# Performance work log

Hardware: AMD Instinct MI355X
Metric: run time of the kernel (lower is better)

The kernel has to match this reference:

```python
import jax, jax.numpy as jnp
import numpy as np

NEG_INF = -1e6

def setup_inputs() -> dict:
    key = jax.random.key(0)
    ks = jax.random.split(key, 7)
    B, Q, K, D, H = 16, 64, 1024, 256, 128
    return {
        "queries": jax.random.normal(ks[0], (B, Q, D), dtype=jnp.float32),
        "keys": jax.random.normal(ks[1], (B, K, D), dtype=jnp.float32),
        "values": jax.random.normal(ks[2], (B, K, D), dtype=jnp.float32),
        "valid_lens": jax.random.randint(ks[3], (B,), 1, K + 1, dtype=jnp.int32),
        "W_q": jax.random.normal(ks[4], (D, H), dtype=jnp.float32) * (1.0 / np.sqrt(D)),
        "W_k": jax.random.normal(ks[5], (D, H), dtype=jnp.float32) * (1.0 / np.sqrt(D)),
        "w_v": jax.random.normal(ks[6], (H,), dtype=jnp.float32) * (1.0 / np.sqrt(H)),
    }

def reference(queries, keys, values, valid_lens, W_q, W_k, w_v):
    # project: [B,Q,H], [B,K,H]
    q = jnp.einsum('bqd,dh->bqh', queries, W_q)
    k = jnp.einsum('bkd,dh->bkh', keys, W_k)
    # broadcast add -> tanh -> score: [B,Q,K]
    features = jnp.tanh(q[:, :, None, :] + k[:, None, :, :])  # [B,Q,K,H]
    scores = jnp.einsum('bqkh,h->bqk', features, w_v)
    # masked softmax over key axis (valid_lens per batch)
    K_len = keys.shape[1]
    mask = jnp.arange(K_len)[None, None, :] < valid_lens[:, None, None]  # [B,1,K]
    scores = jnp.where(mask, scores, NEG_INF)
    attn = jax.nn.softmax(scores, axis=-1)
    # weighted sum of values: [B,Q,Dv]  (dropout p=0 -> identity)
    return jnp.einsum('bqk,bkd->bqd', attn, values)
```

## Files before the change

### kernel.cpp

```cpp
#include <hip/hip_runtime.h>

#define DDIM 256
#define HDIM 128
#define KLEN 1024
#define SCL 2.8853900817779268f

__global__ __launch_bounds__(256) void proj_kernel(
    const float* __restrict__ queries, const float* __restrict__ keys,
    const float* __restrict__ W_q, const float* __restrict__ W_k,
    float* __restrict__ Eq, float* __restrict__ Ek)
{
    __shared__ union {
        float w[64][64];
        float t[64][33];
    } sm;

    int tid = threadIdx.x;
    int hg = tid & 31;
    int rg = tid >> 5;
    int blk = blockIdx.x;

    const float* in; const float* W; int row0, hbase, b = 0, kc0 = 0; bool iskey;
    if (blk < 1024) {
        iskey = true;
        int xcd = blk & 7, s = blk >> 3;
        b = ((s >> 6) << 3) | xcd;
        int r6 = s & 63;
        kc0   = (r6 >> 1) * 32;
        hbase = (r6 & 1) << 6;
        row0  = b * KLEN + kc0;
        in = keys; W = W_k;
    } else {
        iskey = false;
        int qrb = blk - 1024;
        row0  = (qrb >> 1) * 32;
        hbase = (qrb & 1) << 6;
        in = queries; W = W_q;
    }

    float2 acc[4];
    #pragma unroll
    for (int j = 0; j < 4; j++) acc[j] = make_float2(0.f, 0.f);

    for (int dt = 0; dt < DDIM; dt += 64) {
        __syncthreads();
        #pragma unroll
        for (int i = 0; i < 4; i++) {
            int idx = tid + 256 * i;
            int dd = idx >> 4, hl = (idx & 15) << 2;
            *(float4*)(&sm.w[dd][hl]) =
                *(const float4*)(W + (size_t)(dt + dd) * HDIM + hbase + hl);
        }
        __syncthreads();

        #pragma unroll 4
        for (int d4 = 0; d4 < 64; d4 += 4) {
            float2 wr[4];
            #pragma unroll
            for (int dd = 0; dd < 4; dd++)
                wr[dd] = *(const float2*)(&sm.w[d4 + dd][hg << 1]);
            #pragma unroll
            for (int j = 0; j < 4; j++) {
                float4 a = *(const float4*)(in + (size_t)(row0 + rg * 4 + j) * DDIM + dt + d4);
                acc[j].x = fmaf(a.x, wr[0].x, acc[j].x); acc[j].y = fmaf(a.x, wr[0].y, acc[j].y);
                acc[j].x = fmaf(a.y, wr[1].x, acc[j].x); acc[j].y = fmaf(a.y, wr[1].y, acc[j].y);
                acc[j].x = fmaf(a.z, wr[2].x, acc[j].x); acc[j].y = fmaf(a.z, wr[2].y, acc[j].y);
                acc[j].x = fmaf(a.w, wr[3].x, acc[j].x); acc[j].y = fmaf(a.w, wr[3].y, acc[j].y);
            }
        }
    }

    if (!iskey) {
        #pragma unroll
        for (int j = 0; j < 4; j++) {
            float2 o = make_float2(__builtin_amdgcn_exp2f(SCL * acc[j].x),
                                   __builtin_amdgcn_exp2f(SCL * acc[j].y));
            *(float2*)(Eq + (size_t)(row0 + rg * 4 + j) * HDIM + hbase + (hg << 1)) = o;
        }
    } else {
        __syncthreads();
        #pragma unroll
        for (int j = 0; j < 4; j++) {
            sm.t[(hg << 1) + 0][rg * 4 + j] = __builtin_amdgcn_exp2f(SCL * acc[j].x);
            sm.t[(hg << 1) + 1][rg * 4 + j] = __builtin_amdgcn_exp2f(SCL * acc[j].y);
        }
        __syncthreads();
        float* dst = Ek + (size_t)b * HDIM * KLEN + (size_t)hbase * KLEN + kc0;
        #pragma unroll
        for (int i = 0; i < 2; i++) {
            int idx = tid + 256 * i;
            int hh = idx >> 3, c = (idx & 7) << 2;
            float4 o = make_float4(sm.t[hh][c], sm.t[hh][c + 1],
                                   sm.t[hh][c + 2], sm.t[hh][c + 3]);
            *(float4*)(dst + (size_t)hh * KLEN + c) = o;
        }
    }
}

__global__ __launch_bounds__(512) void score_kernel(
    const float* __restrict__ Eq, const float* __restrict__ Ek,
    const float* __restrict__ w_v, const int* __restrict__ valid_lens,
    float* __restrict__ p)
{
    __shared__ float4 eqw[HDIM];
    __shared__ float red0[8], red1[8];

    int tid = threadIdx.x, lane = tid & 63, wav = tid >> 6;
    int blk = blockIdx.x;
    int xcd = blk & 7, s = blk >> 3;
    int b = ((s >= 32) ? 8 : 0) + xcd;
    int qp = s & 31;
    int bq0 = b * 64 + qp * 2;
    int vlen = valid_lens[b];

    if (tid < HDIM) {
        float w2 = -2.0f * w_v[tid];
        eqw[tid] = make_float4(Eq[(size_t)bq0 * HDIM + tid],
                               Eq[(size_t)(bq0 + 1) * HDIM + tid], w2, 0.f);
    }
    __syncthreads();

    int k0 = tid << 1;
    float s00 = -1e30f, s01 = -1e30f, s10 = -1e30f, s11 = -1e30f;
    if (k0 < vlen) {
        const float* ekp = Ek + (size_t)b * HDIM * KLEN + k0;
        float a00 = 0.f, a01 = 0.f, a10 = 0.f, a11 = 0.f;
        #pragma unroll 4
        for (int h = 0; h < HDIM; h++) {
            float2 ek = *(const float2*)(ekp + (size_t)h * KLEN);
            float4 e  = eqw[h];
            a00 = fmaf(e.z, __builtin_amdgcn_rcpf(fmaf(e.x, ek.x, 1.f)), a00);
            a01 = fmaf(e.z, __builtin_amdgcn_rcpf(fmaf(e.x, ek.y, 1.f)), a01);
            a10 = fmaf(e.z, __builtin_amdgcn_rcpf(fmaf(e.y, ek.x, 1.f)), a10);
            a11 = fmaf(e.z, __builtin_amdgcn_rcpf(fmaf(e.y, ek.y, 1.f)), a11);
        }
        s00 = a00; s10 = a10;
        if (k0 + 1 < vlen) { s01 = a01; s11 = a11; }
    }

    float m0 = fmaxf(s00, s01), m1 = fmaxf(s10, s11);
    #pragma unroll
    for (int off = 32; off > 0; off >>= 1) {
        m0 = fmaxf(m0, __shfl_xor(m0, off, 64));
        m1 = fmaxf(m1, __shfl_xor(m1, off, 64));
    }
    if (lane == 0) { red0[wav] = m0; red1[wav] = m1; }
    __syncthreads();
    m0 = red0[0]; m1 = red1[0];
    #pragma unroll
    for (int i = 1; i < 8; i++) {
        m0 = fmaxf(m0, red0[i]);
        m1 = fmaxf(m1, red1[i]);
    }

    float e00 = __expf(s00 - m0), e01 = __expf(s01 - m0);
    float e10 = __expf(s10 - m1), e11 = __expf(s11 - m1);
    float t0 = e00 + e01, t1 = e10 + e11;
    #pragma unroll
    for (int off = 32; off > 0; off >>= 1) {
        t0 += __shfl_xor(t0, off, 64);
        t1 += __shfl_xor(t1, off, 64);
    }
    __syncthreads();
    if (lane == 0) { red0[wav] = t0; red1[wav] = t1; }
    __syncthreads();
    t0 = red0[0]; t1 = red1[0];
    #pragma unroll
    for (int i = 1; i < 8; i++) { t0 += red0[i]; t1 += red1[i]; }
    float inv0 = 1.0f / t0, inv1 = 1.0f / t1;

    float* p0 = p + (size_t)bq0 * KLEN + k0;
    *(float2*)(p0)        = make_float2(e00 * inv0, e01 * inv0);
    *(float2*)(p0 + KLEN) = make_float2(e10 * inv1, e11 * inv1);
}

__global__ __launch_bounds__(256) void av_kernel(
    const float* __restrict__ p, const float* __restrict__ values,
    const int* __restrict__ valid_lens, float* __restrict__ part)
{
    __shared__ float pt[128][10];

    int blk = blockIdx.x;
    int xcd = blk & 7, s = blk >> 3;
    int b = ((s >> 6) << 3) | xcd;
    int r = s & 63, qt = r >> 3, kq = r & 7;
    int tid = threadIdx.x, lane = tid & 63, w = tid >> 6;
    int vlen = valid_lens[b];
    int kbeg = kq << 7;
    int kc = vlen - kbeg; kc = kc < 0 ? 0 : (kc > 128 ? 128 : kc);
    int kc4 = (kc + 3) & ~3;
    int bq0 = b * 64 + qt * 8;

    {
        int q = tid >> 5, k4 = (tid & 31) << 2;
        float4 pv = *(const float4*)(p + (size_t)(bq0 + q) * KLEN + kbeg + k4);
        pt[k4 + 0][q] = pv.x;
        pt[k4 + 1][q] = pv.y;
        pt[k4 + 2][q] = pv.z;
        pt[k4 + 3][q] = pv.w;
    }
    __syncthreads();

    const float* vb = values + ((size_t)b * KLEN + kbeg) * DDIM + (lane << 2);
    float4 a0 = make_float4(0.f, 0.f, 0.f, 0.f);
    float4 a1 = make_float4(0.f, 0.f, 0.f, 0.f);

    for (int k = 0; k < kc4; k += 4) {
        #pragma unroll
        for (int i = 0; i < 4; i++) {
            float2 pp = *(const float2*)(&pt[k + i][w << 1]);
            float4 v  = *(const float4*)(vb + (size_t)(k + i) * DDIM);
            a0.x = fmaf(pp.x, v.x, a0.x); a0.y = fmaf(pp.x, v.y, a0.y);
            a0.z = fmaf(pp.x, v.z, a0.z); a0.w = fmaf(pp.x, v.w, a0.w);
            a1.x = fmaf(pp.y, v.x, a1.x); a1.y = fmaf(pp.y, v.y, a1.y);
            a1.z = fmaf(pp.y, v.z, a1.z); a1.w = fmaf(pp.y, v.w, a1.w);
        }
    }
    float* d0 = part + ((size_t)kq * 1024 + bq0 + (w << 1)) * DDIM + (lane << 2);
    *(float4*)(d0)        = a0;
    *(float4*)(d0 + DDIM) = a1;
}

__global__ __launch_bounds__(256) void combine_kernel(
    const float* __restrict__ part, float* __restrict__ out)
{
    int i = blockIdx.x * 256 + threadIdx.x;
    const float4* p4 = (const float4*)part;
    float4 a = p4[i];
    #pragma unroll
    for (int j = 1; j < 8; j++) {
        float4 v = p4[(size_t)j * 65536 + i];
        a.x += v.x; a.y += v.y; a.z += v.z; a.w += v.w;
    }
    ((float4*)out)[i] = a;
}

extern "C" void kernel_launch(void* const* d_in, const int* in_sizes, int n_in,
                              void* d_out, int out_size, void* d_ws, size_t ws_size,
                              hipStream_t stream) {
    const float* queries    = (const float*)d_in[0];
    const float* keys       = (const float*)d_in[1];
    const float* values     = (const float*)d_in[2];
    const int*   valid_lens = (const int*)d_in[3];
    const float* W_q        = (const float*)d_in[4];
    const float* W_k        = (const float*)d_in[5];
    const float* w_v        = (const float*)d_in[6];

    float* Eq   = (float*)d_ws;
    float* Ek   = Eq + 131072;
    float* p    = Ek + 2097152;
    float* part = Ek;

    proj_kernel<<<1088, 256, 0, stream>>>(queries, keys, W_q, W_k, Eq, Ek);
    score_kernel<<<512, 512, 0, stream>>>(Eq, Ek, w_v, valid_lens, p);
    av_kernel<<<1024, 256, 0, stream>>>(p, values, valid_lens, part);
    combine_kernel<<<256, 256, 0, stream>>>(part, (float*)d_out);
}
```

Before: 166.5 us.

## Retile projection, widen score per-thread work, and unroll AV loop by 32

The projection kernel now stages all of W transposed into padded shared memory once. Each thread computes 8 rows by 2 columns, so there are half as many blocks and no per-64-d reloads or barriers. The score kernel uses 256 threads that each handle 4 keys with float4 loads of Ek, which raises per-thread ILP and cuts block reduction width. The AV loop is unrolled in chunks of 32 rounded up from the valid length. This reads padded zero probabilities but adds more independent loads in flight, trading some wasted rows and register pressure for fewer loop overheads.

```diff
diff --git a/kernel.cpp b/kernel.cpp
--- a/kernel.cpp
+++ b/kernel.cpp
@@ -4,6 +4,7 @@
 #define HDIM 128
 #define KLEN 1024
 #define SCL 2.8853900817779268f
+#define WSTR 260
 
 __global__ __launch_bounds__(256) void proj_kernel(
     const float* __restrict__ queries, const float* __restrict__ keys,
@@ -11,85 +12,94 @@
     float* __restrict__ Eq, float* __restrict__ Ek)
 {
     __shared__ union {
-        float w[64][64];
-        float t[64][33];
+        float w[64 * WSTR];
+        float t[64][68];
     } sm;
 
     int tid = threadIdx.x;
-    int hg = tid & 31;
-    int rg = tid >> 5;
+    int hg  = tid & 31;
+    int rg  = tid >> 5;
     int blk = blockIdx.x;
 
     const float* in; const float* W; int row0, hbase, b = 0, kc0 = 0; bool iskey;
-    if (blk < 1024) {
+    if (blk < 512) {
         iskey = true;
         int xcd = blk & 7, s = blk >> 3;
-        b = ((s >> 6) << 3) | xcd;
-        int r6 = s & 63;
-        kc0   = (r6 >> 1) * 32;
-        hbase = (r6 & 1) << 6;
+        b = ((s >= 32) ? 8 : 0) + xcd;
+        int r = s & 31;
+        kc0   = (r >> 1) * 64;
+        hbase = (r & 1) << 6;
         row0  = b * KLEN + kc0;
         in = keys; W = W_k;
     } else {
         iskey = false;
-        int qrb = blk - 1024;
-        row0  = (qrb >> 1) * 32;
-        hbase = (qrb & 1) << 6;
+        int qi = blk - 512;
+        row0  = (qi >> 1) * 64;
+        hbase = (qi & 1) << 6;
         in = queries; W = W_q;
     }
 
-    float2 acc[4];
-    #pragma unroll
-    for (int j = 0; j < 4; j++) acc[j] = make_float2(0.f, 0.f);
-
-    for (int dt = 0; dt < DDIM; dt += 64) {
-        __syncthreads();
+    {
+        int d4g = tid >> 4;
+        int hl  = (tid & 15) << 2;
         #pragma unroll
         for (int i = 0; i < 4; i++) {
-            int idx = tid + 256 * i;
-            int dd = idx >> 4, hl = (idx & 15) << 2;
-            *(float4*)(&sm.w[dd][hl]) =
-                *(const float4*)(W + (size_t)(dt + dd) * HDIM + hbase + hl);
-        }
-        __syncthreads();
-
-        #pragma unroll 4
-        for (int d4 = 0; d4 < 64; d4 += 4) {
-            float2 wr[4];
-            #pragma unroll
-            for (int dd = 0; dd < 4; dd++)
-                wr[dd] = *(const float2*)(&sm.w[d4 + dd][hg << 1]);
-            #pragma unroll
-            for (int j = 0; j < 4; j++) {
-                float4 a = *(const float4*)(in + (size_t)(row0 + rg * 4 + j) * DDIM + dt + d4);
-                acc[j].x = fmaf(a.x, wr[0].x, acc[j].x); acc[j].y = fmaf(a.x, wr[0].y, acc[j].y);
-                acc[j].x = fmaf(a.y, wr[1].x, acc[j].x); acc[j].y = fmaf(a.y, wr[1].y, acc[j].y);
-                acc[j].x = fmaf(a.z, wr[2].x, acc[j].x); acc[j].y = fmaf(a.z, wr[2].y, acc[j].y);
-                acc[j].x = fmaf(a.w, wr[3].x, acc[j].x); acc[j].y = fmaf(a.w, wr[3].y, acc[j].y);
-            }
+            int d = i * 64 + d4g * 4;
+            float4 g0 = *(const float4*)(W + (size_t)(d + 0) * HDIM + hbase + hl);
+            float4 g1 = *(const float4*)(W + (size_t)(d + 1) * HDIM + hbase + hl);
+            float4 g2 = *(const float4*)(W + (size_t)(d + 2) * HDIM + hbase + hl);
+            float4 g3 = *(const float4*)(W + (size_t)(d + 3) * HDIM + hbase + hl);
+            *(float4*)(&sm.w[(hl + 0) * WSTR + d]) = make_float4(g0.x, g1.x, g2.x, g3.x);
+            *(float4*)(&sm.w[(hl + 1) * WSTR + d]) = make_float4(g0.y, g1.y, g2.y, g3.y);
+            *(float4*)(&sm.w[(hl + 2) * WSTR + d]) = make_float4(g0.z, g1.z, g2.z, g3.z);
+            *(float4*)(&sm.w[(hl + 3) * WSTR + d]) = make_float4(g0.w, g1.w, g2.w, g3.w);
+        }
+    }
+    __syncthreads();
+
+    const float* r0p = in + (size_t)(row0 + rg * 8) * DDIM;
+    const float* wp0 = &sm.w[(size_t)hg * WSTR];
+    const float* wp1 = &sm.w[(size_t)(hg + 32) * WSTR];
+
+    float2 acc[8];
+    #pragma unroll
+    for (int j = 0; j < 8; j++) acc[j] = make_float2(0.f, 0.f);
+
+    #pragma unroll 4
+    for (int d0 = 0; d0 < DDIM; d0 += 4) {
+        float4 w0 = *(const float4*)(wp0 + d0);
+        float4 w1 = *(const float4*)(wp1 + d0);
+        #pragma unroll
+        for (int j = 0; j < 8; j++) {
+            float4 a = *(const float4*)(r0p + (size_t)j * DDIM + d0);
+            acc[j].x = fmaf(a.x, w0.x, acc[j].x); acc[j].y = fmaf(a.x, w1.x, acc[j].y);
+            acc[j].x = fmaf(a.y, w0.y, acc[j].x); acc[j].y = fmaf(a.y, w1.y, acc[j].y);
+            acc[j].x = fmaf(a.z, w0.z, acc[j].x); acc[j].y = fmaf(a.z, w1.z, acc[j].y);
+            acc[j].x = fmaf(a.w, w0.w, acc[j].x); acc[j].y = fmaf(a.w, w1.w, acc[j].y);
         }
     }
 
     if (!iskey) {
         #pragma unroll
-        for (int j = 0; j < 4; j++) {
-            float2 o = make_float2(__builtin_amdgcn_exp2f(SCL * acc[j].x),
-                                   __builtin_amdgcn_exp2f(SCL * acc[j].y));
-            *(float2*)(Eq + (size_t)(row0 + rg * 4 + j) * HDIM + hbase + (hg << 1)) = o;
+        for (int j = 0; j < 8; j++) {
+            float* er = Eq + (size_t)(row0 + rg * 8 + j) * HDIM + hbase;
+            er[hg]      = __builtin_amdgcn_exp2f(SCL * acc[j].x);
+            er[hg + 32] = __builtin_amdgcn_exp2f(SCL * acc[j].y);
         }
     } else {
         __syncthreads();
         #pragma unroll
-        for (int j = 0; j < 4; j++) {
-            sm.t[(hg << 1) + 0][rg * 4 + j] = __builtin_amdgcn_exp2f(SCL * acc[j].x);
-            sm.t[(hg << 1) + 1][rg * 4 + j] = __builtin_amdgcn_exp2f(SCL * acc[j].y);
+        for (int j = 0; j < 8; j++) {
+            int kl = rg * 8 + j;
+            sm.t[hg][kl]      = __builtin_amdgcn_exp2f(SCL * acc[j].x);
+            sm.t[hg + 32][kl] = __builtin_amdgcn_exp2f(SCL * acc[j].y);
         }
         __syncthreads();
         float* dst = Ek + (size_t)b * HDIM * KLEN + (size_t)hbase * KLEN + kc0;
         #pragma unroll
-        for (int i = 0; i < 2; i++) {
-            int idx = tid + 256 * i;
-            int hh = idx >> 3, c = (idx & 7) << 2;
+        for (int ii = 0; ii < 4; ii++) {
+            int i2 = tid + 256 * ii;
+            int hh = i2 >> 4, c = (i2 & 15) << 2;
             float4 o = make_float4(sm.t[hh][c], sm.t[hh][c + 1],
                                    sm.t[hh][c + 2], sm.t[hh][c + 3]);
             *(float4*)(dst + (size_t)hh * KLEN + c) = o;
@@ -97,13 +107,13 @@
     }
 }
 
-__global__ __launch_bounds__(512) void score_kernel(
+__global__ __launch_bounds__(256) void score_kernel(
     const float* __restrict__ Eq, const float* __restrict__ Ek,
     const float* __restrict__ w_v, const int* __restrict__ valid_lens,
     float* __restrict__ p)
 {
     __shared__ float4 eqw[HDIM];
-    __shared__ float red0[8], red1[8];
+    __shared__ float red0[4], red1[4];
 
     int tid = threadIdx.x, lane = tid & 63, wav = tid >> 6;
     int blk = blockIdx.x;
@@ -113,32 +123,43 @@
     int bq0 = b * 64 + qp * 2;
     int vlen = valid_lens[b];
 
-    if (tid < HDIM) {
-        float w2 = -2.0f * w_v[tid];
+    if (tid < HDIM)
         eqw[tid] = make_float4(Eq[(size_t)bq0 * HDIM + tid],
-                               Eq[(size_t)(bq0 + 1) * HDIM + tid], w2, 0.f);
-    }
-    __syncthreads();
-
-    int k0 = tid << 1;
-    float s00 = -1e30f, s01 = -1e30f, s10 = -1e30f, s11 = -1e30f;
+                               Eq[(size_t)(bq0 + 1) * HDIM + tid],
+                               -2.0f * w_v[tid], 0.f);
+    __syncthreads();
+
+    int k0 = tid << 2;
+    float a[8];
+    #pragma unroll
+    for (int i = 0; i < 8; i++) a[i] = 0.f;
+
     if (k0 < vlen) {
         const float* ekp = Ek + (size_t)b * HDIM * KLEN + k0;
-        float a00 = 0.f, a01 = 0.f, a10 = 0.f, a11 = 0.f;
-        #pragma unroll 4
+        #pragma unroll 16
         for (int h = 0; h < HDIM; h++) {
-            float2 ek = *(const float2*)(ekp + (size_t)h * KLEN);
+            float4 ek = *(const float4*)(ekp + (size_t)h * KLEN);
             float4 e  = eqw[h];
-            a00 = fmaf(e.z, __builtin_amdgcn_rcpf(fmaf(e.x, ek.x, 1.f)), a00);
-            a01 = fmaf(e.z, __builtin_amdgcn_rcpf(fmaf(e.x, ek.y, 1.f)), a01);
-            a10 = fmaf(e.z, __builtin_amdgcn_rcpf(fmaf(e.y, ek.x, 1.f)), a10);
-            a11 = fmaf(e.z, __builtin_amdgcn_rcpf(fmaf(e.y, ek.y, 1.f)), a11);
-        }
-        s00 = a00; s10 = a10;
-        if (k0 + 1 < vlen) { s01 = a01; s11 = a11; }
-    }
-
-    float m0 = fmaxf(s00, s01), m1 = fmaxf(s10, s11);
+            a[0] = fmaf(e.z, __builtin_amdgcn_rcpf(fmaf(e.x, ek.x, 1.f)), a[0]);
+            a[1] = fmaf(e.z, __builtin_amdgcn_rcpf(fmaf(e.x, ek.y, 1.f)), a[1]);
+            a[2] = fmaf(e.z, __builtin_amdgcn_rcpf(fmaf(e.x, ek.z, 1.f)), a[2]);
+            a[3] = fmaf(e.z, __builtin_amdgcn_rcpf(fmaf(e.x, ek.w, 1.f)), a[3]);
+            a[4] = fmaf(e.z, __builtin_amdgcn_rcpf(fmaf(e.y, ek.x, 1.f)), a[4]);
+            a[5] = fmaf(e.z, __builtin_amdgcn_rcpf(fmaf(e.y, ek.y, 1.f)), a[5]);
+            a[6] = fmaf(e.z, __builtin_amdgcn_rcpf(fmaf(e.y, ek.z, 1.f)), a[6]);
+            a[7] = fmaf(e.z, __builtin_amdgcn_rcpf(fmaf(e.y, ek.w, 1.f)), a[7]);
+        }
+    }
+    float s0[4], s1[4];
+    #pragma unroll
+    for (int i = 0; i < 4; i++) {
+        bool v = (k0 + i) < vlen;
+        s0[i] = v ? a[i] : -1e30f;
+        s1[i] = v ? a[4 + i] : -1e30f;
+    }
+
+    float m0 = fmaxf(fmaxf(s0[0], s0[1]), fmaxf(s0[2], s0[3]));
+    float m1 = fmaxf(fmaxf(s1[0], s1[1]), fmaxf(s1[2], s1[3]));
     #pragma unroll
     for (int off = 32; off > 0; off >>= 1) {
         m0 = fmaxf(m0, __shfl_xor(m0, off, 64));
@@ -146,16 +167,16 @@
     }
     if (lane == 0) { red0[wav] = m0; red1[wav] = m1; }
     __syncthreads();
-    m0 = red0[0]; m1 = red1[0];
-    #pragma unroll
-    for (int i = 1; i < 8; i++) {
-        m0 = fmaxf(m0, red0[i]);
-        m1 = fmaxf(m1, red1[i]);
-    }
-
-    float e00 = __expf(s00 - m0), e01 = __expf(s01 - m0);
-    float e10 = __expf(s10 - m1), e11 = __expf(s11 - m1);
-    float t0 = e00 + e01, t1 = e10 + e11;
+    m0 = fmaxf(fmaxf(red0[0], red0[1]), fmaxf(red0[2], red0[3]));
+    m1 = fmaxf(fmaxf(red1[0], red1[1]), fmaxf(red1[2], red1[3]));
+
+    float e0[4], e1[4], t0 = 0.f, t1 = 0.f;
+    #pragma unroll
+    for (int i = 0; i < 4; i++) {
+        e0[i] = __expf(s0[i] - m0);
+        e1[i] = __expf(s1[i] - m1);
+        t0 += e0[i]; t1 += e1[i];
+    }
     #pragma unroll
     for (int off = 32; off > 0; off >>= 1) {
         t0 += __shfl_xor(t0, off, 64);
@@ -164,14 +185,12 @@
     __syncthreads();
     if (lane == 0) { red0[wav] = t0; red1[wav] = t1; }
     __syncthreads();
-    t0 = red0[0]; t1 = red1[0];
-    #pragma unroll
-    for (int i = 1; i < 8; i++) { t0 += red0[i]; t1 += red1[i]; }
-    float inv0 = 1.0f / t0, inv1 = 1.0f / t1;
+    float inv0 = 1.0f / (red0[0] + red0[1] + red0[2] + red0[3]);
+    float inv1 = 1.0f / (red1[0] + red1[1] + red1[2] + red1[3]);
 
     float* p0 = p + (size_t)bq0 * KLEN + k0;
-    *(float2*)(p0)        = make_float2(e00 * inv0, e01 * inv0);
-    *(float2*)(p0 + KLEN) = make_float2(e10 * inv1, e11 * inv1);
+    *(float4*)(p0)        = make_float4(e0[0] * inv0, e0[1] * inv0, e0[2] * inv0, e0[3] * inv0);
+    *(float4*)(p0 + KLEN) = make_float4(e1[0] * inv1, e1[1] * inv1, e1[2] * inv1, e1[3] * inv1);
 }
 
 __global__ __launch_bounds__(256) void av_kernel(
@@ -188,7 +207,6 @@
     int vlen = valid_lens[b];
     int kbeg = kq << 7;
     int kc = vlen - kbeg; kc = kc < 0 ? 0 : (kc > 128 ? 128 : kc);
-    int kc4 = (kc + 3) & ~3;
     int bq0 = b * 64 + qt * 8;
 
     {
@@ -205,11 +223,13 @@
     float4 a0 = make_float4(0.f, 0.f, 0.f, 0.f);
     float4 a1 = make_float4(0.f, 0.f, 0.f, 0.f);
 
-    for (int k = 0; k < kc4; k += 4) {
-        #pragma unroll
-        for (int i = 0; i < 4; i++) {
-            float2 pp = *(const float2*)(&pt[k + i][w << 1]);
-            float4 v  = *(const float4*)(vb + (size_t)(k + i) * DDIM);
+    int kcc = (kc + 31) & ~31;
+    for (int kt = 0; kt < kcc; kt += 32) {
+        #pragma unroll
+        for (int k2 = 0; k2 < 32; k2++) {
+            int k = kt + k2;
+            float2 pp = *(const float2*)(&pt[k][w << 1]);
+            float4 v  = *(const float4*)(vb + (size_t)k * DDIM);
             a0.x = fmaf(pp.x, v.x, a0.x); a0.y = fmaf(pp.x, v.y, a0.y);
             a0.z = fmaf(pp.x, v.z, a0.z); a0.w = fmaf(pp.x, v.w, a0.w);
             a1.x = fmaf(pp.y, v.x, a1.x); a1.y = fmaf(pp.y, v.y, a1.y);
@@ -251,8 +271,8 @@
     float* p    = Ek + 2097152;
     float* part = Ek;
 
-    proj_kernel<<<1088, 256, 0, stream>>>(queries, keys, W_q, W_k, Eq, Ek);
-    score_kernel<<<512, 512, 0, stream>>>(Eq, Ek, w_v, valid_lens, p);
+    proj_kernel<<<544, 256, 0, stream>>>(queries, keys, W_q, W_k, Eq, Ek);
+    score_kernel<<<512, 256, 0, stream>>>(Eq, Ek, w_v, valid_lens, p);
     av_kernel<<<1024, 256, 0, stream>>>(p, values, valid_lens, part);
     combine_kernel<<<256, 256, 0, stream>>>(part, (float*)d_out);
 }
```

After: 180.3 us. 1.08x slower.
